# Optimization experiments

Measured on AMD Instinct MI355X. Metric: run time of the kernel, lower is better.

## Reference

```python
import jax, jax.numpy as jnp
import numpy as np

KERNEL_SIZE = 3
PADDING = KERNEL_SIZE // 2
EPS = 1e-12  # matches torch F.normalize default eps


def setup_inputs() -> dict:
    key = jax.random.key(0)
    k1, k2 = jax.random.split(key)
    query_feat = jax.random.normal(k1, (8, 512, 64, 64), dtype=jnp.float32)
    memory_bank = jax.random.normal(k2, (32, 512, 64, 64), dtype=jnp.float32)
    return {"query_feat": query_feat, "memory_bank": memory_bank}


def _l2_normalize(x, axis):
    n = jnp.sqrt(jnp.sum(x * x, axis=axis, keepdims=True))
    return x / jnp.maximum(n, EPS)


def reference(query_feat, memory_bank):
    # query_feat: (B, C, H, W); memory_bank: (M, C, H, W)
    b, c, h, w = query_feat.shape
    qn = _l2_normalize(query_feat, axis=1)
    mn = _l2_normalize(memory_bank, axis=1)
    # zero-pad memory spatially (matches F.unfold zero padding)
    mp = jnp.pad(mn, ((0, 0), (0, 0), (PADDING, PADDING), (PADDING, PADDING)))
    # Correlation via shifted dot-products over the K^2 window offsets,
    # keeping a running max instead of materializing (M, C, K^2, H, W).
    sim_max = None
    for di in range(KERNEL_SIZE):
        for dj in range(KERNEL_SIZE):
            shifted = mp[:, :, di:di + h, dj:dj + w]  # (M, C, H, W)
            s = jnp.einsum('mchw,bchw->bmhw', shifted, qn)  # cosine sims
            sim_max = s if sim_max is None else jnp.maximum(sim_max, s)
    pairwise = jnp.maximum(sim_max, 0.0)          # clamp(min=0), (B, M, H, W)
    group = jnp.mean(pairwise, axis=1)            # mean aggregation over M
    anomaly_map = 1.0 - group[:, None, :, :]      # (B, 1, H, W)
    return anomaly_map
```

## Files before the change

kernel.cpp:

```cpp
#include <hip/hip_runtime.h>

#define B_ 8
#define M_ 32
#define C_ 512
#define H_ 64
#define W_ 64
#define HW 4096
#define NKT 16
#define KC 32
#define CKG 128
#define TW 4
#define TH 2
#define NPOS 8
#define PW 6
#define PH 4
#define NPM 24
#define HP 66
#define WP 66
#define HPWP (HP*WP)

typedef __attribute__((ext_vector_type(8))) short short8;
typedef __attribute__((ext_vector_type(4))) float float4v;

static __device__ __forceinline__ unsigned pk_bf16(float lo, float hi) {
    unsigned r;
    asm("v_cvt_pk_bf16_f32 %0, %1, %2" : "=v"(r) : "v"(lo), "v"(hi));
    return r;
}

static __device__ __forceinline__ void load_lds16(const short* g, short* l) {
    __builtin_amdgcn_global_load_lds((const __attribute__((address_space(1))) void*)g,
                                     (__attribute__((address_space(3))) void*)l, 16, 0, 0);
}

__global__ void zero_norms(float* __restrict__ p) {
    int i = blockIdx.x * 256 + threadIdx.x;
    ((float4v*)p)[i] = (float4v){0.f, 0.f, 0.f, 0.f};
}

__global__ __launch_bounds__(512, 8)
void prep_kernel(const float* __restrict__ Q, const float* __restrict__ Mb,
                 short* __restrict__ qT, short* __restrict__ mT,
                 float* __restrict__ nq, float* __restrict__ nm) {
    __shared__ unsigned buf[2][2176];

    const int tid = threadIdx.x;
    const bool isq = (blockIdx.x < 1024);
    const int g  = isq ? (int)blockIdx.x : (int)blockIdx.x - 1024;
    const int pr  = g >> 8;
    const int h   = (g >> 2) & 63;
    const int ktg = g & 3;
    const float* base = (isq ? Q : Mb) + (size_t)(pr * 2) * C_ * HW + h * W_;

    const int w4 = tid & 15, cpair = (tid >> 4) & 15, limg = tid >> 8;
    const float* lsrc = base + (size_t)limg * C_ * HW + (size_t)(ktg * CKG + cpair * 2) * HW + w4 * 4;
    unsigned* wA = &buf[0][limg * 1088 + cpair];
    unsigned* wB = &buf[1][limg * 1088 + cpair];
    const int ckq = tid & 3, rimg = (tid >> 2) & 1, rw = tid >> 3;
    const unsigned* rA = &buf[0][rimg * 1088 + rw * 17 + ckq * 4];
    const unsigned* rB = &buf[1][rimg * 1088 + rw * 17 + ckq * 4];

    float4v ssq = {0.f, 0.f, 0.f, 0.f};
    float4v a0, a1, b0, b1, c0, c1, d0, d1;

#define LOADP(ch, r0, r1) { const float* p_ = lsrc + (size_t)(ch) * 32 * HW; \
                            r0 = *(const float4v*)p_; r1 = *(const float4v*)(p_ + HW); }
#define WRITEP(wb, r0, r1) { ssq += r0 * r0 + r1 * r1; \
    wb[(w4*4+0)*17] = pk_bf16(r0[0], r1[0]); wb[(w4*4+1)*17] = pk_bf16(r0[1], r1[1]); \
    wb[(w4*4+2)*17] = pk_bf16(r0[2], r1[2]); wb[(w4*4+3)*17] = pk_bf16(r0[3], r1[3]); }
#define STOREP(ch, rb) { union { unsigned u[4]; short8 s; } o_; \
    o_.u[0] = rb[0]; o_.u[1] = rb[1]; o_.u[2] = rb[2]; o_.u[3] = rb[3]; \
    const int kt_ = ktg * 4 + (ch); short* dst_; \
    if (isq) dst_ = qT + (((size_t)kt_ * HW + h * 64 + rw) * B_ + pr * 2 + rimg) * KC + ckq * 8; \
    else     dst_ = mT + (((size_t)kt_ * HPWP + (size_t)(h + 1) * WP + rw + 1) * M_ + pr * 2 + rimg) * KC + ckq * 8; \
    *(short8*)dst_ = o_.s; }

    LOADP(0, a0, a1);
    WRITEP(wA, a0, a1);
    LOADP(1, b0, b1);
    __syncthreads();
    LOADP(2, c0, c1);
    STOREP(0, rA);
    WRITEP(wB, b0, b1);
    __syncthreads();
    LOADP(3, d0, d1);
    STOREP(1, rB);
    WRITEP(wA, c0, c1);
    __syncthreads();
    STOREP(2, rA);
    WRITEP(wB, d0, d1);
    __syncthreads();
    STOREP(3, rB);
    float* red = (float*)&buf[0][0];
    *(float4v*)&red[(limg * 16 + cpair) * 64 + w4 * 4] = ssq;
    __syncthreads();

    if (tid < 128) {
        int im_ = tid >> 6, w = tid & 63;
        float t = 0.f;
        #pragma unroll
        for (int cp = 0; cp < 16; ++cp) t += red[(im_ * 16 + cp) * 64 + w];
        atomicAdd(&(isq ? nq : nm)[(size_t)(pr * 2 + im_) * HW + h * 64 + w], t);
    }

    if (!isq) {
        short8 z = (short8){0, 0, 0, 0, 0, 0, 0, 0};
        if (tid < 64) {
            int e = tid & 7, kk = (tid >> 3) & 3, c = tid >> 5;
            int kt = ktg * 4 + kk;
            *(short8*)(mT + ((size_t)kt * HPWP + (size_t)(h + 1) * WP + (c ? 65 : 0)) * (M_ * KC)
                       + pr * 64 + e * 8) = z;
        }
        if (h == 0 || h == 63) {
            int row = (h == 0) ? 0 : 65;
            for (int j = tid; j < 66 * 4 * 8; j += 512) {
                int e = j & 7, kk = (j >> 3) & 3, cell = j >> 5;
                int kt = ktg * 4 + kk;
                *(short8*)(mT + ((size_t)kt * HPWP + (size_t)row * WP + cell) * (M_ * KC)
                           + pr * 64 + e * 8) = z;
            }
        }
    }
#undef LOADP
#undef WRITEP
#undef STOREP
}

__global__ __launch_bounds__(512)
void gcm_kernel(const short* __restrict__ qT, const short* __restrict__ mT,
                const float* __restrict__ nq, const float* __restrict__ nm,
                float* __restrict__ out) {
    __shared__ __align__(16) short m_lds[NPM * M_ * KC];
    __shared__ __align__(16) short q_lds[NPOS * 16 * KC];

    const int tid = threadIdx.x;
    const int bx = blockIdx.x & 15, by = blockIdx.x >> 4;
    const int w0 = bx * TW, h0 = by * TH;
    const int wid = tid >> 6, lane = tid & 63;
    const int lw = wid & 3, lh = wid >> 2;
    const int col = lane & 15, kg = lane >> 4;
    const int mypos = lh * TW + lw;
    const int gh = h0 + lh, gw = w0 + lw;

    {
        short8 z = (short8){0, 0, 0, 0, 0, 0, 0, 0};
        *(short8*)&q_lds[tid * 8] = z;
    }

    float4v acc[9][2];
    #pragma unroll
    for (int d = 0; d < 9; ++d)
        #pragma unroll
        for (int hf = 0; hf < 2; ++hf)
            acc[d][hf] = (float4v){0.f, 0.f, 0.f, 0.f};

    for (int kt = 0; kt < NKT; ++kt) {
        __syncthreads();
        if (tid < 256) {
            int chunk = tid & 3, b = (tid >> 2) & 7, pidx = tid >> 5;
            int qh = h0 + (pidx >> 2), qw = w0 + (pidx & 3);
            const short* src = qT + (((size_t)kt * HW + qh * W_ + qw) * B_ + b) * KC + chunk * 8;
            *(short8*)&q_lds[pidx * 512 + b * KC + chunk * 8] = *(const short8*)src;
        }
        for (int j = wid; j < NPM * 2; j += 8) {
            int pm = j >> 1, half = j & 1;
            int ph = pm / PW, pw = pm % PW;
            size_t pos2 = (size_t)(h0 + ph) * WP + (w0 + pw);
            const short* gsrc = mT + ((size_t)kt * HPWP + pos2) * (M_ * KC)
                              + half * 512 + (size_t)lane * 8;
            short* ldst = m_lds + pm * 1024 + half * 512;
            load_lds16(gsrc, ldst);
        }
        __syncthreads();
        short8 aq = *(const short8*)&q_lds[mypos * 512 + col * KC + kg * 8];
        #pragma unroll
        for (int dh = 0; dh < 3; ++dh)
            #pragma unroll
            for (int dw = 0; dw < 3; ++dw) {
                const int pm = (lh + dh) * PW + (lw + dw);
                #pragma unroll
                for (int hf = 0; hf < 2; ++hf) {
                    short8 bm = *(const short8*)&m_lds[pm * 1024 + (hf * 16 + col) * KC + kg * 8];
                    acc[dh * 3 + dw][hf] =
                        __builtin_amdgcn_mfma_f32_16x16x32_bf16(aq, bm, acc[dh * 3 + dw][hf], 0, 0, 0);
                }
            }
    }

    float iq[4];
    #pragma unroll
    for (int r = 0; r < 4; ++r) {
        float ss = nq[(size_t)((kg & 1) * 4 + r) * HW + gh * W_ + gw];
        iq[r] = 1.0f / fmaxf(sqrtf(ss), 1e-12f);
    }
    float im[2][9];
    #pragma unroll
    for (int dh = 0; dh < 3; ++dh)
        #pragma unroll
        for (int dw = 0; dw < 3; ++dw) {
            int hh = min(63, max(0, gh + dh - 1));
            int ww = min(63, max(0, gw + dw - 1));
            #pragma unroll
            for (int hf = 0; hf < 2; ++hf) {
                float ss = nm[(size_t)(hf * 16 + col) * HW + hh * W_ + ww];
                im[hf][dh * 3 + dw] = 1.0f / fmaxf(sqrtf(ss), 1e-12f);
            }
        }
    float res[4];
    #pragma unroll
    for (int r = 0; r < 4; ++r) {
        float v0 = -1e30f, v1 = -1e30f;
        #pragma unroll
        for (int d = 0; d < 9; ++d) {
            v0 = fmaxf(v0, acc[d][0][r] * im[0][d]);
            v1 = fmaxf(v1, acc[d][1][r] * im[1][d]);
        }
        res[r] = fmaxf(v0 * iq[r], 0.f) + fmaxf(v1 * iq[r], 0.f);
    }
    #pragma unroll
    for (int mask = 1; mask < 16; mask <<= 1)
        #pragma unroll
        for (int r = 0; r < 4; ++r)
            res[r] += __shfl_xor(res[r], mask);

    if (col == 0 && kg < 2) {
        #pragma unroll
        for (int r = 0; r < 4; ++r) {
            int b = kg * 4 + r;
            out[(size_t)b * HW + gh * W_ + gw] = 1.0f - res[r] * (1.0f / M_);
        }
    }
}

extern "C" void kernel_launch(void* const* d_in, const int* in_sizes, int n_in,
                              void* d_out, int out_size, void* d_ws, size_t ws_size,
                              hipStream_t stream) {
    const float* Q  = (const float*)d_in[0];
    const float* Mb = (const float*)d_in[1];
    float* out = (float*)d_out;

    const size_t MT_SHORTS = (size_t)NKT * HPWP * M_ * KC;
    const size_t QT_SHORTS = (size_t)NKT * HW * B_ * KC;
    short* mT = (short*)d_ws;
    short* qT = mT + MT_SHORTS;
    float* nq = (float*)(qT + QT_SHORTS);
    float* nm = nq + B_ * HW;

    zero_norms<<<160, 256, 0, stream>>>(nq);
    prep_kernel<<<5120, 512, 0, stream>>>(Q, Mb, qT, mT, nq, nm);
    gcm_kernel<<<512, 512, 0, stream>>>(qT, mT, nq, nm, out);
}
```

Baseline: 153.6 us.

## Replace atomic norm accumulation with partial-sum buffers and issue all prep loads upfront

The separate zero-init kernel and the atomicAdd of squared norms are dropped. Each of the four channel groups now writes its own partial sum-of-squares plane, and the consumer kernel adds the four partials when it loads norms. The prep kernel also issues all four channel-chunk global loads before the LDS transpose stages, with launch bounds relaxed from 8 to 4 waves per SIMD to make room for the extra registers. This removes a kernel launch and atomic traffic and adds memory-level parallelism in prep, at the cost of four times more norm reads in gcm and possibly lower occupancy in prep.

```diff
diff --git a/kernel.cpp b/kernel.cpp
--- a/kernel.cpp
+++ b/kernel.cpp
@@ -33,15 +33,10 @@
                                      (__attribute__((address_space(3))) void*)l, 16, 0, 0);
 }
 
-__global__ void zero_norms(float* __restrict__ p) {
-    int i = blockIdx.x * 256 + threadIdx.x;
-    ((float4v*)p)[i] = (float4v){0.f, 0.f, 0.f, 0.f};
-}
-
-__global__ __launch_bounds__(512, 8)
+__global__ __launch_bounds__(512, 4)
 void prep_kernel(const float* __restrict__ Q, const float* __restrict__ Mb,
                  short* __restrict__ qT, short* __restrict__ mT,
-                 float* __restrict__ nq, float* __restrict__ nm) {
+                 float* __restrict__ nqp, float* __restrict__ nmp) {
     __shared__ unsigned buf[2][2176];
 
     const int tid = threadIdx.x;
@@ -76,31 +71,35 @@
     *(short8*)dst_ = o_.s; }
 
     LOADP(0, a0, a1);
+    LOADP(1, b0, b1);
+    LOADP(2, c0, c1);
+    LOADP(3, d0, d1);
+
     WRITEP(wA, a0, a1);
-    LOADP(1, b0, b1);
-    __syncthreads();
-    LOADP(2, c0, c1);
-    STOREP(0, rA);
-    WRITEP(wB, b0, b1);
-    __syncthreads();
-    LOADP(3, d0, d1);
-    STOREP(1, rB);
-    WRITEP(wA, c0, c1);
-    __syncthreads();
-    STOREP(2, rA);
-    WRITEP(wB, d0, d1);
+    __syncthreads();
+    STOREP(0, rA); WRITEP(wB, b0, b1);
+    __syncthreads();
+    STOREP(1, rB); WRITEP(wA, c0, c1);
+    __syncthreads();
+    STOREP(2, rA); WRITEP(wB, d0, d1);
     __syncthreads();
     STOREP(3, rB);
-    float* red = (float*)&buf[0][0];
-    *(float4v*)&red[(limg * 16 + cpair) * 64 + w4 * 4] = ssq;
+    {
+        float* red = (float*)&buf[0][0];
+        *(float4v*)&red[(limg * 16 + cpair) * 64 + w4 * 4] = ssq;
+    }
     __syncthreads();
 
     if (tid < 128) {
+        const float* red = (const float*)&buf[0][0];
         int im_ = tid >> 6, w = tid & 63;
         float t = 0.f;
         #pragma unroll
         for (int cp = 0; cp < 16; ++cp) t += red[(im_ * 16 + cp) * 64 + w];
-        atomicAdd(&(isq ? nq : nm)[(size_t)(pr * 2 + im_) * HW + h * 64 + w], t);
+        const int img = pr * 2 + im_;
+        const int pix = h * 64 + w;
+        if (isq) nqp[((size_t)ktg * B_ + img) * HW + pix] = t;
+        else     nmp[((size_t)ktg * M_ + img) * HW + pix] = t;
     }
 
     if (!isq) {
@@ -128,7 +127,7 @@
 
 __global__ __launch_bounds__(512)
 void gcm_kernel(const short* __restrict__ qT, const short* __restrict__ mT,
-                const float* __restrict__ nq, const float* __restrict__ nm,
+                const float* __restrict__ nqp, const float* __restrict__ nmp,
                 float* __restrict__ out) {
     __shared__ __align__(16) short m_lds[NPM * M_ * KC];
     __shared__ __align__(16) short q_lds[NPOS * 16 * KC];
@@ -190,7 +189,11 @@
     float iq[4];
     #pragma unroll
     for (int r = 0; r < 4; ++r) {
-        float ss = nq[(size_t)((kg & 1) * 4 + r) * HW + gh * W_ + gw];
+        int b = (kg & 1) * 4 + r;
+        float ss = 0.f;
+        #pragma unroll
+        for (int k = 0; k < 4; ++k)
+            ss += nqp[((size_t)k * B_ + b) * HW + gh * W_ + gw];
         iq[r] = 1.0f / fmaxf(sqrtf(ss), 1e-12f);
     }
     float im[2][9];
@@ -202,7 +205,11 @@
             int ww = min(63, max(0, gw + dw - 1));
             #pragma unroll
             for (int hf = 0; hf < 2; ++hf) {
-                float ss = nm[(size_t)(hf * 16 + col) * HW + hh * W_ + ww];
+                int mi = hf * 16 + col;
+                float ss = 0.f;
+                #pragma unroll
+                for (int k = 0; k < 4; ++k)
+                    ss += nmp[((size_t)k * M_ + mi) * HW + hh * W_ + ww];
                 im[hf][dh * 3 + dw] = 1.0f / fmaxf(sqrtf(ss), 1e-12f);
             }
         }
@@ -243,10 +250,9 @@
     const size_t QT_SHORTS = (size_t)NKT * HW * B_ * KC;
     short* mT = (short*)d_ws;
     short* qT = mT + MT_SHORTS;
-    float* nq = (float*)(qT + QT_SHORTS);
-    float* nm = nq + B_ * HW;
-
-    zero_norms<<<160, 256, 0, stream>>>(nq);
-    prep_kernel<<<5120, 512, 0, stream>>>(Q, Mb, qT, mT, nq, nm);
-    gcm_kernel<<<512, 512, 0, stream>>>(qT, mT, nq, nm, out);
-}
+    float* nqp = (float*)(qT + QT_SHORTS);
+    float* nmp = nqp + 4 * B_ * HW;
+
+    prep_kernel<<<5120, 512, 0, stream>>>(Q, Mb, qT, mT, nqp, nmp);
+    gcm_kernel<<<512, 512, 0, stream>>>(qT, mT, nqp, nmp, out);
+}
```

After: 176.0 us. 14.6% more time.
